# Kernel optimization log

Measured on AMD Instinct MI355X. Metric: run time of the kernel, lower is better.

## Reference

```python
import jax, jax.numpy as jnp
import numpy as np

GRID_ROWS, GRID_COLS = 7, 10
GRID_SIZE = GRID_ROWS * GRID_COLS  # 70
CONTEXT_SIZE = 24
STATE_SIZE = GRID_SIZE + CONTEXT_SIZE  # 94
H = 128  # LSTM_HIDDEN


def setup_inputs() -> dict:
    key = jax.random.key(0)
    ks = jax.random.split(key, 16)
    B, T = 1024, 128
    inp = {
        'states_seq': jax.random.normal(ks[0], (B, T, STATE_SIZE), jnp.float32),
        'actions_seq': jax.random.randint(ks[1], (B, T), 0, 4).astype(jnp.int32),
        # conv params (OIHW)
        'conv1_w': jax.random.normal(ks[2], (16, 1, 3, 3), jnp.float32) * 0.3,
        'conv1_b': jnp.zeros((16,), jnp.float32),
        'conv2_w': jax.random.normal(ks[3], (32, 16, 3, 3), jnp.float32) * 0.08,
        'conv2_b': jnp.zeros((32,), jnp.float32),
        # dense params (out, in) like torch Linear
        'grid_fc_w': jax.random.normal(ks[4], (128, 32 * GRID_SIZE), jnp.float32) * 0.02,
        'grid_fc_b': jnp.zeros((128,), jnp.float32),
        'ctx_fc_w': jax.random.normal(ks[5], (64, CONTEXT_SIZE), jnp.float32) * 0.2,
        'ctx_fc_b': jnp.zeros((64,), jnp.float32),
        'trunk_w': jax.random.normal(ks[6], (128, 192), jnp.float32) * 0.07,
        'trunk_b': jnp.zeros((128,), jnp.float32),
        # LSTM params
        'W_ih': jax.random.normal(ks[7], (4 * H, 128), jnp.float32) * 0.09,
        'b_ih': jnp.zeros((4 * H,), jnp.float32),
        'W_hh': jax.random.normal(ks[8], (4 * H, H), jnp.float32) * 0.09,
        # heads
        'actor_w': jax.random.uniform(ks[9], (4, H), jnp.float32, -0.01, 0.01),
        'actor_b': jnp.zeros((4,), jnp.float32),
        'critic_w': jax.random.uniform(ks[10], (1, H), jnp.float32, -0.01, 0.01),
        'critic_b': jnp.zeros((1,), jnp.float32),
    }
    return inp


def _forward(states_seq, actions_seq, conv1_w, conv1_b, conv2_w, conv2_b,
             grid_fc_w, grid_fc_b, ctx_fc_w, ctx_fc_b, trunk_w, trunk_b,
             W_ih, b_ih, W_hh, actor_w, actor_b, critic_w, critic_b):
    B, T, _ = states_seq.shape
    x = states_seq.reshape(-1, STATE_SIZE)                  # (N, 94)
    grid = x[:, :GRID_SIZE].reshape(-1, 1, GRID_ROWS, GRID_COLS)
    ctx = x[:, GRID_SIZE:]
    g = jax.lax.conv_general_dilated(grid, conv1_w, (1, 1), 'SAME',
                                     dimension_numbers=('NCHW', 'OIHW', 'NCHW'))
    g = jax.nn.relu(g + conv1_b[None, :, None, None])
    g = jax.lax.conv_general_dilated(g, conv2_w, (1, 1), 'SAME',
                                     dimension_numbers=('NCHW', 'OIHW', 'NCHW'))
    g = jax.nn.relu(g + conv2_b[None, :, None, None])
    g = g.reshape(g.shape[0], -1)                           # (N, 2240)
    g = jax.nn.relu(g @ grid_fc_w.T + grid_fc_b)            # (N, 128)
    c = jax.nn.relu(ctx @ ctx_fc_w.T + ctx_fc_b)            # (N, 64)
    trunk = jax.nn.relu(jnp.concatenate([g, c], -1) @ trunk_w.T + trunk_b)
    trunk = trunk.reshape(B, T, 128)

    # LSTM: precompute input-to-gate GEMM for all timesteps, scan over time
    gates_x = jnp.einsum('btd,gd->tbg', trunk, W_ih) + b_ih  # (T, B, 4H)

    def step(carry, gx):
        h, cst = carry
        gates = gx + h @ W_hh.T
        i, f, gg, o = jnp.split(gates, 4, axis=-1)
        i, f, o = jax.nn.sigmoid(i), jax.nn.sigmoid(f), jax.nn.sigmoid(o)
        gg = jnp.tanh(gg)
        cst = f * cst + i * gg
        h = o * jnp.tanh(cst)
        return (h, cst), h

    h0 = jnp.zeros((B, H), trunk.dtype)
    _, hs = jax.lax.scan(step, (h0, h0), gates_x)            # hs: (T, B, H)
    h_flat = jnp.transpose(hs, (1, 0, 2)).reshape(B * T, H)

    logits = h_flat @ actor_w.T + actor_b                    # (N, 4)
    values = (h_flat @ critic_w.T + critic_b)[:, 0]          # (N,)
    logp = jax.nn.log_softmax(logits, axis=-1)
    a = actions_seq.reshape(-1)
    log_probs = jnp.take_along_axis(logp, a[:, None].astype(jnp.int32), axis=-1)[:, 0]
    entropy = -jnp.sum(jnp.exp(logp) * logp, axis=-1)
    return log_probs, values, entropy


def reference(states_seq, actions_seq, conv1_w, conv1_b, conv2_w, conv2_b,
              grid_fc_w, grid_fc_b, ctx_fc_w, ctx_fc_b, trunk_w, trunk_b,
              W_ih, b_ih, W_hh, actor_w, actor_b, critic_w, critic_b):
    return _forward(states_seq, actions_seq, conv1_w, conv1_b, conv2_w, conv2_b,
                    grid_fc_w, grid_fc_b, ctx_fc_w, ctx_fc_b, trunk_w, trunk_b,
                    W_ih, b_ih, W_hh, actor_w, actor_b, critic_w, critic_b)
```

## Files before the change

### kernel.cpp

```cpp
#include <hip/hip_runtime.h>
#include <hip/hip_bf16.h>

typedef unsigned int  u32;
typedef unsigned short u16;
typedef unsigned long long u64;
typedef __attribute__((ext_vector_type(8))) short bf16x8;
typedef __attribute__((ext_vector_type(4))) float f32x4;

#define B_   1024
#define T_   128
#define NBT  (B_*T_)
#define CH   16384
#define NCH  8

#define WG_OFF   0
#define WT_OFF   286720
#define WIH_OFF  311296
#define W2_OFF   376832
#define W1C_OFF  381952
#define CVT_TOTAL 382464

#define TRUNK_OFF (1ull<<20)
#define H_OFF     (36ull<<20)
#define CTX_OFF   (72ull<<20)
#define C2A_OFF   (92ull<<20)
#define C2B_OFF   (C2A_OFF + 74ull*1024*1024)

__device__ __forceinline__ u16 f2bf(float f){
  __hip_bfloat16 h = __float2bfloat16(f);
  return *reinterpret_cast<u16*>(&h);
}
__device__ __forceinline__ float bf2f(u16 u){ return __uint_as_float((u32)u << 16); }
__device__ __forceinline__ float sigm(float x){ return 1.f / (1.f + __expf(-x)); }
__device__ __forceinline__ float tanh_f(float x){ return 2.f / (1.f + __expf(-2.f*x)) - 1.f; }

__device__ __forceinline__ void bar_lds() {
  __builtin_amdgcn_sched_barrier(0);
  asm volatile("s_waitcnt lgkmcnt(0)" ::: "memory");
  __builtin_amdgcn_s_barrier();
  __builtin_amdgcn_sched_barrier(0);
}

__global__ void k_cvt(const float* __restrict__ gfw, const float* __restrict__ tw,
                      const float* __restrict__ wih, const float* __restrict__ c2w,
                      const float* __restrict__ c1w, u16* __restrict__ wsb) {
  int i = blockIdx.x * 256 + threadIdx.x;
  if (i >= CVT_TOTAL) return;
  float v;
  if (i < WT_OFF) {
    int o = i / 2240; int k = i - o*2240;
    int pos = k >> 5, ch = k & 31;
    v = gfw[o*2240 + ch*70 + pos];
  }
  else if (i < WIH_OFF)  v = tw[i - WT_OFF];
  else if (i < W2_OFF)   v = wih[i - WIH_OFF];
  else if (i < W1C_OFF) {
    int j = i - W2_OFF; int co = j / 160; int k = j - co*160;
    int tap = k >> 4; int ci = k & 15;
    v = (tap < 9) ? c2w[co*144 + ci*9 + tap] : 0.f;
  } else {
    int j = i - W1C_OFF; int ch = j >> 5; int k = j & 31;
    v = (k < 9) ? c1w[ch*9 + k] : 0.f;
  }
  wsb[i] = f2bf(v);
}

__device__ void conv_body(char* smem,
    const float* __restrict__ states_c,
    const float* __restrict__ c1b, const float* __restrict__ c2b,
    const float* __restrict__ cfw, const float* __restrict__ cfb,
    const u16* __restrict__ wsb,
    u16* __restrict__ c2buf, u16* __restrict__ ctx_c, int blk)
{
  float (*s_st)[96] = (float(*)[96])smem;
  u16* act1 = (u16*)(smem + 3072);

  const int tid  = threadIdx.x;
  const int lane = tid & 63;
  const int w    = tid >> 6;
  const int arow = lane & 15;
  const int grp  = lane >> 4;
  const int g0   = blk * 64;

  bf16x8 Bc1 = *(const bf16x8*)(wsb + W1C_OFF + arow*32 + grp*8);
  bf16x8 b2f[5][2];
  #pragma unroll
  for (int p = 0; p < 5; p++)
    #pragma unroll
    for (int nt = 0; nt < 2; nt++)
      b2f[p][nt] = *(const bf16x8*)(wsb + W2_OFF + (nt*16 + arow)*160 + p*32 + grp*8);
  float c1bv[4], c2bv0[4], c2bv1[4];
  #pragma unroll
  for (int r = 0; r < 4; r++) {
    c1bv[r]  = c1b[grp*4 + r];
    c2bv0[r] = c2b[grp*4 + r];
    c2bv1[r] = c2b[16 + grp*4 + r];
  }
  const float cfbr = cfb[lane];
  float cfwr[24];
  #pragma unroll
  for (int k = 0; k < 24; k++) cfwr[k] = cfw[lane*24 + k];

  const int sst_s = (tid*2)/94, sst_c = (tid*2)%94;

  if (tid < 376) {
    float2 v = *(const float2*)(states_c + (size_t)g0*94 + tid*2);
    *(float2*)&s_st[sst_s][sst_c] = v;
  }
  for (int i = tid; i < 608; i += 512) {
    int s = i / 76; int r = i - s*76; int hi2 = r >> 1; int h = r & 1;
    int hp;
    if (hi2 < 12)      hp = hi2;
    else if (hi2 < 24) hp = 96 + (hi2 - 12);
    else if (hi2 < 31) hp = (hi2 - 23) * 12;
    else               hp = (hi2 - 30) * 12 + 11;
    u32 a = (u32)((s*108 + hp)*32 + h*16) ^ (u32)((hp & 7) << 4);
    *(uint4*)(act1 ? (char*)act1 + a : 0) = (uint4){0,0,0,0};
  }
  bar_lds();

  const bf16x8 zv = {0,0,0,0,0,0,0,0};

  for (int g = 0; g < 8; g++) {
    const int m0 = g0 + g*8;
    float2 npre;
    const bool haspre = (g < 7) && (tid < 376);
    if (haspre)
      npre = *(const float2*)(states_c + (size_t)(m0 + 8)*94 + tid*2);

    for (int mt = w; mt < 35; mt += 8) {
      int row = mt*16 + arow;
      int s = (int)(((u32)row * 59919u) >> 22); int pos = row - s*70;
      int y = (int)(((u32)pos * 6554u) >> 16);  int x = pos - y*10;
      bf16x8 pf = zv;
      if (grp == 0) {
        const float* gs = &s_st[s][0];
        #pragma unroll
        for (int t = 0; t < 8; t++) {
          int dy = t/3, dx = t - (t/3)*3;
          int yy = y + dy - 1, xx = x + dx - 1;
          bool ok = (yy >= 0) & (yy < 7) & (xx >= 0) & (xx < 10);
          float v = gs[ok ? yy*10 + xx : 0];
          pf[t] = (short)f2bf(ok ? v : 0.f);
        }
      } else if (grp == 1) {
        int yy = y + 1, xx = x + 1;
        bool ok = (yy < 7) & (xx < 10);
        float v = s_st[s][ok ? yy*10 + xx : 0];
        pf[0] = (short)f2bf(ok ? v : 0.f);
      }
      f32x4 acc = __builtin_amdgcn_mfma_f32_16x16x32_bf16(Bc1, pf, (f32x4){0.f,0.f,0.f,0.f}, 0, 0, 0);
      int hp = (y+1)*12 + (x+1);
      u16 q0 = f2bf(fmaxf(acc[0] + c1bv[0], 0.f));
      u16 q1 = f2bf(fmaxf(acc[1] + c1bv[1], 0.f));
      u16 q2 = f2bf(fmaxf(acc[2] + c1bv[2], 0.f));
      u16 q3 = f2bf(fmaxf(acc[3] + c1bv[3], 0.f));
      u64 pk = (u64)q0 | ((u64)q1 << 16) | ((u64)q2 << 32) | ((u64)q3 << 48);
      u32 wa = (u32)(((s*108 + hp)*16 + grp*4)*2) ^ (u32)((hp & 7) << 4);
      *(u64*)((char*)act1 + wa) = pk;
    }
    bar_lds();

    for (int mt = w; mt < 35; mt += 8) {
      int row = mt*16 + arow;
      int s = (int)(((u32)row * 59919u) >> 22); int pos = row - s*70;
      int y = (int)(((u32)pos * 6554u) >> 16);  int x = pos - y*10;
      f32x4 acc0 = {0.f,0.f,0.f,0.f}, acc1 = {0.f,0.f,0.f,0.f};
      #pragma unroll
      for (int p = 0; p < 5; p++) {
        int tap = p*2 + (grp >> 1); if (tap > 8) tap = 8;
        int dy = (tap * 11) >> 5; int dx = tap - dy*3;
        int hp = (y + dy)*12 + (x + dx);
        u32 ra = (u32)(((s*108 + hp)*16 + (grp & 1)*8)*2) ^ (u32)((hp & 7) << 4);
        bf16x8 bv = *(const bf16x8*)((const char*)act1 + ra);
        acc0 = __builtin_amdgcn_mfma_f32_16x16x32_bf16(b2f[p][0], bv, acc0, 0, 0, 0);
        acc1 = __builtin_amdgcn_mfma_f32_16x16x32_bf16(b2f[p][1], bv, acc1, 0, 0, 0);
      }
      {
        u16 q0 = f2bf(fmaxf(acc0[0] + c2bv0[0], 0.f));
        u16 q1 = f2bf(fmaxf(acc0[1] + c2bv0[1], 0.f));
        u16 q2 = f2bf(fmaxf(acc0[2] + c2bv0[2], 0.f));
        u16 q3 = f2bf(fmaxf(acc0[3] + c2bv0[3], 0.f));
        u64 pk = (u64)q0 | ((u64)q1 << 16) | ((u64)q2 << 32) | ((u64)q3 << 48);
        *(u64*)(c2buf + (size_t)(m0 + s)*2240 + pos*32 + grp*4) = pk;
      }
      {
        u16 q0 = f2bf(fmaxf(acc1[0] + c2bv1[0], 0.f));
        u16 q1 = f2bf(fmaxf(acc1[1] + c2bv1[1], 0.f));
        u16 q2 = f2bf(fmaxf(acc1[2] + c2bv1[2], 0.f));
        u16 q3 = f2bf(fmaxf(acc1[3] + c2bv1[3], 0.f));
        u64 pk = (u64)q0 | ((u64)q1 << 16) | ((u64)q2 << 32) | ((u64)q3 << 48);
        *(u64*)(c2buf + (size_t)(m0 + s)*2240 + pos*32 + 16 + grp*4) = pk;
      }
    }
    {
      float a = cfbr;
      #pragma unroll
      for (int k = 0; k < 24; k++) a = fmaf(cfwr[k], s_st[w][70 + k], a);
      ctx_c[(size_t)(m0 + w)*64 + lane] = f2bf(fmaxf(a, 0.f));
    }

    if (g < 7) {
      bar_lds();
      if (haspre) *(float2*)&s_st[sst_s][sst_c] = npre;
      bar_lds();
    }
  }
}

__device__ void gemm_body(char* smem,
    const u16* __restrict__ c2buf, const u16* __restrict__ ctx_c,
    const float* __restrict__ gfb, const float* __restrict__ tbv,
    const u16* __restrict__ wsb, u16* __restrict__ trunk_ws,
    int nbase, int blk)
{
  u16* s_b = (u16*)smem;
  u16* s_g = (u16*)(smem + 36864);

  const int tid  = threadIdx.x;
  const int lane = tid & 63;
  const int w    = tid >> 6;
  const int arow = lane & 15;
  const int grp  = lane >> 4;
  const int wm   = w & 3;
  const int wn   = w >> 2;
  const int m0   = blk * 64;

  float gfbv[4], tbvv[4];
  #pragma unroll
  for (int q = 0; q < 4; q++) {
    gfbv[q] = gfb[(wn*4 + q)*16 + arow];
    tbvv[q] = tbv[(wn*4 + q)*16 + arow];
  }

  const int srow = tid >> 2, sseg = (tid & 3) * 16;
  const u16* wg = wsb + WG_OFF;
  const u16* ap = c2buf + (size_t)(m0 + wm*16 + arow) * 2240 + grp*8;

  {
    const u16* src = wg + (size_t)srow*2240 + sseg;
    *(uint4*)&s_b[srow*72 + sseg]     = *(const uint4*)src;
    *(uint4*)&s_b[srow*72 + sseg + 8] = *(const uint4*)(src + 8);
  }
  bf16x8 aC0 = *(const bf16x8*)(ap);
  bf16x8 aC1 = *(const bf16x8*)(ap + 32);
  bf16x8 aN0 = *(const bf16x8*)(ap + 64);
  bf16x8 aN1 = *(const bf16x8*)(ap + 96);
  f32x4 acc[4];
  #pragma unroll
  for (int q = 0; q < 4; q++) acc[q] = (f32x4){0.f,0.f,0.f,0.f};
  __syncthreads();

  for (int kp = 0; kp < 35; kp++) {
    uint4 b0v, b1v;
    if (kp < 34) {
      const u16* src = wg + (size_t)srow*2240 + (kp+1)*64 + sseg;
      b0v = *(const uint4*)src;
      b1v = *(const uint4*)(src + 8);
    }
    bf16x8 aF0 = aN0, aF1 = aN1;
    if (kp < 33) {
      aF0 = *(const bf16x8*)(ap + (size_t)(kp+2)*64);
      aF1 = *(const bf16x8*)(ap + (size_t)(kp+2)*64 + 32);
    }
    const u16* sb = &s_b[(kp & 1)*9216];
    #pragma unroll
    for (int q = 0; q < 4; q++) {
      bf16x8 bv0 = *(const bf16x8*)&sb[((wn*4 + q)*16 + arow)*72 + grp*8];
      acc[q] = __builtin_amdgcn_mfma_f32_16x16x32_bf16(aC0, bv0, acc[q], 0, 0, 0);
    }
    #pragma unroll
    for (int q = 0; q < 4; q++) {
      bf16x8 bv1 = *(const bf16x8*)&sb[((wn*4 + q)*16 + arow)*72 + 32 + grp*8];
      acc[q] = __builtin_amdgcn_mfma_f32_16x16x32_bf16(aC1, bv1, acc[q], 0, 0, 0);
    }
    if (kp < 34) {
      *(uint4*)&s_b[((kp+1) & 1)*9216 + srow*72 + sseg]     = b0v;
      *(uint4*)&s_b[((kp+1) & 1)*9216 + srow*72 + sseg + 8] = b1v;
    }
    aC0 = aN0; aC1 = aN1; aN0 = aF0; aN1 = aF1;
    bar_lds();
  }

  #pragma unroll
  for (int q = 0; q < 4; q++)
    #pragma unroll
    for (int r = 0; r < 4; r++)
      s_g[(wm*16 + grp*4 + r)*204 + (wn*4 + q)*16 + arow] = f2bf(fmaxf(acc[q][r] + gfbv[q], 0.f));
  {
    int row = tid >> 3, seg = (tid & 7) * 8;
    uint4 c0 = *(const uint4*)(ctx_c + (size_t)(m0 + row)*64 + seg);
    *(uint4*)&s_g[row*204 + 128 + seg] = c0;
  }
  bar_lds();

  f32x4 tacc[4];
  #pragma unroll
  for (int q = 0; q < 4; q++) tacc[q] = (f32x4){0.f,0.f,0.f,0.f};
  #pragma unroll
  for (int ks = 0; ks < 6; ks++) {
    bf16x8 av = *(const bf16x8*)&s_g[(wm*16 + arow)*204 + ks*32 + grp*8];
    #pragma unroll
    for (int q = 0; q < 4; q++) {
      bf16x8 bv = *(const bf16x8*)(wsb + WT_OFF + (size_t)((wn*4 + q)*16 + arow)*192 + ks*32 + grp*8);
      tacc[q] = __builtin_amdgcn_mfma_f32_16x16x32_bf16(av, bv, tacc[q], 0, 0, 0);
    }
  }
  bar_lds();
  #pragma unroll
  for (int q = 0; q < 4; q++)
    #pragma unroll
    for (int r = 0; r < 4; r++)
      s_g[(wm*16 + grp*4 + r)*204 + (wn*4 + q)*16 + arow] = f2bf(fmaxf(tacc[q][r] + tbvv[q], 0.f));
  bar_lds();

  {
    const int t0 = (nbase + m0) & 127;
    const int bb = (nbase + m0) >> 7;
    int row = tid >> 3, seg = (tid & 7) * 16;
    #pragma unroll
    for (int j = 0; j < 2; j++) {
      uint4 v = *(const uint4*)&s_g[row*204 + seg + j*8];
      *(uint4*)(trunk_ws + ((size_t)(t0 + row)*B_ + bb)*128 + seg + j*8) = v;
    }
  }
}

__global__ __launch_bounds__(512, 2) void k_fused(
    const float* __restrict__ states,
    const float* __restrict__ c1b, const float* __restrict__ c2b,
    const float* __restrict__ cfw, const float* __restrict__ cfb,
    const float* __restrict__ gfb, const float* __restrict__ tbv,
    const u16* __restrict__ wsb,
    u16* __restrict__ c2a, u16* __restrict__ c2bb,
    u16* __restrict__ ctxg, u16* __restrict__ trunk_ws,
    int i, int nconv)
{
  __shared__ __align__(16) char smem[62976];
  if ((int)blockIdx.x < nconv) {
    const float* st_c = states + (size_t)i * CH * 94;
    u16* c2w_  = (i & 1) ? c2bb : c2a;
    u16* ctx_c = ctxg + (size_t)i * CH * 64;
    conv_body(smem, st_c, c1b, c2b, cfw, cfb, wsb, c2w_, ctx_c, blockIdx.x);
  } else {
    const int c = i - 1;
    const u16* c2r   = (c & 1) ? c2bb : c2a;
    const u16* ctx_c = ctxg + (size_t)c * CH * 64;
    gemm_body(smem, c2r, ctx_c, gfb, tbv, wsb, trunk_ws, c*CH, blockIdx.x - nconv);
  }
}

__global__ __launch_bounds__(512, 1) void k_lstm(
    const u16* __restrict__ trunk_ws, const float* __restrict__ whh,
    const float* __restrict__ wih, const float* __restrict__ bih,
    u16* __restrict__ h_ws)
{
  __shared__ __align__(16) u16 s_h[2][16*136];
  __shared__ __align__(16) u16 s_tk[3][4*136];

  const int tid  = threadIdx.x;
  const int lane = tid & 63;
  const int w    = tid >> 6;
  const int arow = lane & 15;
  const int grp  = lane >> 4;
  const int b0   = blockIdx.x * 4;

  bf16x8 Bv[4][4], Bw[4][4];
  float bihv[4];
  #pragma unroll
  for (int j = 0; j < 4; j++) {
    const int row = j*128 + w*16 + arow;
    bihv[j] = bih[row];
    #pragma unroll
    for (int ks = 0; ks < 4; ks++) {
      const float* s1 = whh + (size_t)row*128 + ks*32 + grp*8;
      const float* s2 = wih + (size_t)row*128 + ks*32 + grp*8;
      float4 a0 = *(const float4*)s1, a1 = *(const float4*)(s1 + 4);
      float4 b0v = *(const float4*)s2, b1v = *(const float4*)(s2 + 4);
      bf16x8 t1, t2;
      t1[0]=(short)f2bf(a0.x); t1[1]=(short)f2bf(a0.y); t1[2]=(short)f2bf(a0.z); t1[3]=(short)f2bf(a0.w);
      t1[4]=(short)f2bf(a1.x); t1[5]=(short)f2bf(a1.y); t1[6]=(short)f2bf(a1.z); t1[7]=(short)f2bf(a1.w);
      t2[0]=(short)f2bf(b0v.x); t2[1]=(short)f2bf(b0v.y); t2[2]=(short)f2bf(b0v.z); t2[3]=(short)f2bf(b0v.w);
      t2[4]=(short)f2bf(b1v.x); t2[5]=(short)f2bf(b1v.y); t2[6]=(short)f2bf(b1v.z); t2[7]=(short)f2bf(b1v.w);
      Bv[j][ks] = t1; Bw[j][ks] = t2;
    }
  }

  for (int i = tid; i < 2*16*136; i += 512) ((u16*)s_h)[i] = 0;

  const int prow = tid >> 4, pseg = (tid & 15) * 8;
  if (tid < 64) {
    #pragma unroll
    for (int s = 0; s < 3; s++)
      *(uint4*)&s_tk[s][prow*136 + pseg] =
          *(const uint4*)(trunk_ws + ((size_t)s*B_ + b0 + prow)*128 + pseg);
  }
  uint4 P0 = {0,0,0,0};
  if (tid < 64)
    P0 = *(const uint4*)(trunk_ws + ((size_t)3*B_ + b0 + prow)*128 + pseg);

  float cst = 0.f;
  __syncthreads();

  f32x4 xA[4];
  #pragma unroll
  for (int j = 0; j < 4; j++) xA[j] = (f32x4){0.f,0.f,0.f,0.f};
  #pragma unroll
  for (int ks = 0; ks < 4; ks++) {
    bf16x8 av = *(const bf16x8*)&s_tk[0][(arow & 3)*136 + ks*32 + grp*8];
    #pragma unroll
    for (int j = 0; j < 4; j++)
      xA[j] = __builtin_amdgcn_mfma_f32_16x16x32_bf16(av, Bw[j][ks], xA[j], 0, 0, 0);
  }

  for (int t = 0; t < T_; t++) {
    const int p = t & 1;

    uint4 P1 = {0,0,0,0};
    if ((t + 4 < T_) && tid < 64)
      P1 = *(const uint4*)(trunk_ws + ((size_t)(t+4)*B_ + b0 + prow)*128 + pseg);

    if (t > 0 && tid < 64) {
      uint4 hv = *(const uint4*)&s_h[p][prow*136 + pseg];
      *(uint4*)(h_ws + ((size_t)(t-1)*B_ + b0 + prow)*128 + pseg) = hv;
    }

    f32x4 racc[4], xB[4];
    #pragma unroll
    for (int j = 0; j < 4; j++) { racc[j] = (f32x4){0.f,0.f,0.f,0.f}; xB[j] = (f32x4){0.f,0.f,0.f,0.f}; }
    #pragma unroll
    for (int ks = 0; ks < 4; ks++) {
      bf16x8 av = *(const bf16x8*)&s_h[p][arow*136 + ks*32 + grp*8];
      #pragma unroll
      for (int j = 0; j < 4; j++)
        racc[j] = __builtin_amdgcn_mfma_f32_16x16x32_bf16(av, Bv[j][ks], racc[j], 0, 0, 0);
    }
    {
      const u16* tk = &s_tk[(t+1) % 3][0];
      #pragma unroll
      for (int ks = 0; ks < 4; ks++) {
        bf16x8 av = *(const bf16x8*)&tk[(arow & 3)*136 + ks*32 + grp*8];
        #pragma unroll
        for (int j = 0; j < 4; j++)
          xB[j] = __builtin_amdgcn_mfma_f32_16x16x32_bf16(av, Bw[j][ks], xB[j], 0, 0, 0);
      }
    }

    float g4[4];
    #pragma unroll
    for (int j = 0; j < 4; j++) {
      float s0 = racc[j][0] + xA[j][0];
      float s1 = racc[j][1] + xA[j][1];
      float s2 = racc[j][2] + xA[j][2];
      float s3 = racc[j][3] + xA[j][3];
      float t0v = __shfl(s0, arow);
      float t1v = __shfl(s1, arow);
      float t2v = __shfl(s2, arow);
      float t3v = __shfl(s3, arow);
      g4[j] = (grp == 0) ? t0v : (grp == 1) ? t1v : (grp == 2) ? t2v : t3v;
    }

    {
      float xi = g4[0] + bihv[0];
      float xf = g4[1] + bihv[1];
      float xg = g4[2] + bihv[2];
      float xo = g4[3] + bihv[3];
      float I = sigm(xi), F = sigm(xf), O = sigm(xo), G = tanh_f(xg);
      cst = F*cst + I*G;
      float hvv = O * tanh_f(cst);
      s_h[1-p][grp*136 + w*16 + arow] = f2bf(hvv);
    }

    if ((t + 3 < T_) && tid < 64)
      *(uint4*)&s_tk[t % 3][prow*136 + pseg] = P0;
    P0 = P1;
    #pragma unroll
    for (int j = 0; j < 4; j++) xA[j] = xB[j];
    bar_lds();
  }

  if (tid < 64) {
    uint4 hv = *(const uint4*)&s_h[T_ & 1][prow*136 + pseg];
    *(uint4*)(h_ws + ((size_t)(T_-1)*B_ + b0 + prow)*128 + pseg) = hv;
  }
}

__global__ __launch_bounds__(256, 1) void k_heads(
    const u16* __restrict__ h_ws, const int* __restrict__ actions,
    const float* __restrict__ aw, const float* __restrict__ ab,
    const float* __restrict__ cw, const float* __restrict__ cb,
    float* __restrict__ out)
{
  const int tid  = threadIdx.x;
  const int lane = tid & 63;
  const int w    = tid >> 6;
  const int arow = lane & 15;
  const int grp  = lane >> 4;

  bf16x8 Ah[4];
  #pragma unroll
  for (int ks = 0; ks < 4; ks++) {
    bf16x8 v = {0,0,0,0,0,0,0,0};
    if (arow < 4) {
      const float* src = aw + arow*128 + ks*32 + grp*8;
      #pragma unroll
      for (int j = 0; j < 8; j++) v[j] = (short)f2bf(src[j]);
    } else if (arow == 4) {
      const float* src = cw + ks*32 + grp*8;
      #pragma unroll
      for (int j = 0; j < 8; j++) v[j] = (short)f2bf(src[j]);
    }
    Ah[ks] = v;
  }
  const float ab0=ab[0], ab1=ab[1], ab2=ab[2], ab3=ab[3], cb0=cb[0];

  #pragma unroll
  for (int g = 0; g < 4; g++) {
    int m0 = (blockIdx.x*4 + w)*64 + g*16;
    int t  = m0 >> 10; int bb = m0 & 1023;
    f32x4 acc = {0.f,0.f,0.f,0.f};
    #pragma unroll
    for (int ks = 0; ks < 4; ks++) {
      bf16x8 bv = *(const bf16x8*)(h_ws + ((size_t)t*B_ + bb + arow)*128 + ks*32 + grp*8);
      acc = __builtin_amdgcn_mfma_f32_16x16x32_bf16(Ah[ks], bv, acc, 0, 0, 0);
    }
    float cr = __shfl_xor(acc[0], 16);
    if (grp == 0) {
      float L0 = acc[0] + ab0, L1 = acc[1] + ab1, L2 = acc[2] + ab2, L3 = acc[3] + ab3;
      float Lv = cr + cb0;
      float mm = fmaxf(fmaxf(L0, L1), fmaxf(L2, L3));
      float e0 = __expf(L0-mm), e1 = __expf(L1-mm), e2 = __expf(L2-mm), e3 = __expf(L3-mm);
      float S = e0+e1+e2+e3; float lse = __logf(S);
      float p0=L0-mm-lse, p1=L1-mm-lse, p2=L2-mm-lse, p3=L3-mm-lse;
      int n = (bb + arow)*T_ + t;
      int a = actions[n];
      float lpa = (a==0)?p0:(a==1)?p1:(a==2)?p2:p3;
      float ent = -(e0*p0 + e1*p1 + e2*p2 + e3*p3) / S;
      out[n] = lpa; out[NBT + n] = Lv; out[2*NBT + n] = ent;
    }
  }
}

extern "C" void kernel_launch(void* const* d_in, const int* in_sizes, int n_in,
                              void* d_out, int out_size, void* d_ws, size_t ws_size,
                              hipStream_t stream) {
  const float* states = (const float*)d_in[0];
  const int*   actions= (const int*)  d_in[1];
  const float* c1w = (const float*)d_in[2];
  const float* c1b = (const float*)d_in[3];
  const float* c2w = (const float*)d_in[4];
  const float* c2b = (const float*)d_in[5];
  const float* gfw = (const float*)d_in[6];
  const float* gfb = (const float*)d_in[7];
  const float* cfw = (const float*)d_in[8];
  const float* cfb = (const float*)d_in[9];
  const float* tw  = (const float*)d_in[10];
  const float* tbv = (const float*)d_in[11];
  const float* wih = (const float*)d_in[12];
  const float* bih = (const float*)d_in[13];
  const float* whh = (const float*)d_in[14];
  const float* aw  = (const float*)d_in[15];
  const float* ab  = (const float*)d_in[16];
  const float* cw  = (const float*)d_in[17];
  const float* cb  = (const float*)d_in[18];
  float* out = (float*)d_out;

  u16* wsb   = (u16*)d_ws;
  u16* trunk = (u16*)((char*)d_ws + TRUNK_OFF);
  u16* h_ws  = (u16*)((char*)d_ws + H_OFF);
  u16* ctxg  = (u16*)((char*)d_ws + CTX_OFF);
  u16* c2a   = (u16*)((char*)d_ws + C2A_OFF);
  u16* c2bb  = (u16*)((char*)d_ws + C2B_OFF);

  k_cvt<<<(CVT_TOTAL + 255)/256, 256, 0, stream>>>(gfw, tw, wih, c2w, c1w, wsb);

  for (int i = 0; i <= NCH; i++) {
    const int nconv = (i < NCH) ? (CH/64) : 0;
    const int ngemm = (i > 0)   ? (CH/64) : 0;
    k_fused<<<nconv + ngemm, 512, 0, stream>>>(states, c1b, c2b, cfw, cfb,
                                               gfb, tbv, wsb, c2a, c2bb,
                                               ctxg, trunk, i, nconv);
  }
  k_lstm<<<B_/4, 512, 0, stream>>>(trunk, whh, wih, bih, h_ws);
  k_heads<<<512, 256, 0, stream>>>(h_ws, actions, aw, ab, cw, cb, out);
}
```

Before: 784.7 us.

## Fuse conv and grid GEMM per block, enlarge chunks, pad LSTM LDS rows

Replaces the software-pipelined launch sequence, where each launch ran the conv for chunk i and the GEMM for chunk i-1 in separate blocks using double-buffered conv2 scratch, with a kernel in which each block runs conv and then immediately runs the GEMM on its own rows. A threadfence and syncthreads separate the two phases. Chunks double in size, giving fewer launches, and the conv2 buffer becomes single. The LSTM shared-memory row stride changes from 136 to 144 elements, which alters the LDS bank mapping. The design assumes each block's GEMM reads only the conv output that same block produced; otherwise the result is racy. The conv2 intermediate, now twice as large per chunk, may also be less likely to stay in cache.

```diff
diff --git a/kernel.cpp b/kernel.cpp
--- a/kernel.cpp
+++ b/kernel.cpp
@@ -10,8 +10,8 @@
 #define B_   1024
 #define T_   128
 #define NBT  (B_*T_)
-#define CH   16384
-#define NCH  8
+#define CHUNK 32768
+#define NCHUNK 4
 
 #define WG_OFF   0
 #define WT_OFF   286720
@@ -23,8 +23,7 @@
 #define TRUNK_OFF (1ull<<20)
 #define H_OFF     (36ull<<20)
 #define CTX_OFF   (72ull<<20)
-#define C2A_OFF   (92ull<<20)
-#define C2B_OFF   (C2A_OFF + 74ull*1024*1024)
+#define C2_OFF    (92ull<<20)
 
 __device__ __forceinline__ u16 f2bf(float f){
   __hip_bfloat16 h = __float2bfloat16(f);
@@ -115,7 +114,7 @@
     else if (hi2 < 31) hp = (hi2 - 23) * 12;
     else               hp = (hi2 - 30) * 12 + 11;
     u32 a = (u32)((s*108 + hp)*32 + h*16) ^ (u32)((hp & 7) << 4);
-    *(uint4*)(act1 ? (char*)act1 + a : 0) = (uint4){0,0,0,0};
+    *(uint4*)((char*)act1 + a) = (uint4){0,0,0,0};
   }
   bar_lds();
 
@@ -326,28 +325,22 @@
   }
 }
 
-__global__ __launch_bounds__(512, 2) void k_fused(
+__global__ __launch_bounds__(512, 2) void k_cg(
     const float* __restrict__ states,
     const float* __restrict__ c1b, const float* __restrict__ c2b,
     const float* __restrict__ cfw, const float* __restrict__ cfb,
     const float* __restrict__ gfb, const float* __restrict__ tbv,
     const u16* __restrict__ wsb,
-    u16* __restrict__ c2a, u16* __restrict__ c2bb,
-    u16* __restrict__ ctxg, u16* __restrict__ trunk_ws,
-    int i, int nconv)
+    u16* __restrict__ c2g, u16* __restrict__ ctxg,
+    u16* __restrict__ trunk_ws, int c)
 {
   __shared__ __align__(16) char smem[62976];
-  if ((int)blockIdx.x < nconv) {
-    const float* st_c = states + (size_t)i * CH * 94;
-    u16* c2w_  = (i & 1) ? c2bb : c2a;
-    u16* ctx_c = ctxg + (size_t)i * CH * 64;
-    conv_body(smem, st_c, c1b, c2b, cfw, cfb, wsb, c2w_, ctx_c, blockIdx.x);
-  } else {
-    const int c = i - 1;
-    const u16* c2r   = (c & 1) ? c2bb : c2a;
-    const u16* ctx_c = ctxg + (size_t)c * CH * 64;
-    gemm_body(smem, c2r, ctx_c, gfb, tbv, wsb, trunk_ws, c*CH, blockIdx.x - nconv);
-  }
+  const float* st_c  = states + (size_t)c * CHUNK * 94;
+  u16*         ctx_c = ctxg + (size_t)c * CHUNK * 64;
+  conv_body(smem, st_c, c1b, c2b, cfw, cfb, wsb, c2g, ctx_c, blockIdx.x);
+  __threadfence();
+  __syncthreads();
+  gemm_body(smem, c2g, ctx_c, gfb, tbv, wsb, trunk_ws, c*CHUNK, blockIdx.x);
 }
 
 __global__ __launch_bounds__(512, 1) void k_lstm(
@@ -355,8 +348,8 @@
     const float* __restrict__ wih, const float* __restrict__ bih,
     u16* __restrict__ h_ws)
 {
-  __shared__ __align__(16) u16 s_h[2][16*136];
-  __shared__ __align__(16) u16 s_tk[3][4*136];
+  __shared__ __align__(16) u16 s_h[2][16*144];
+  __shared__ __align__(16) u16 s_tk[3][4*144];
 
   const int tid  = threadIdx.x;
   const int lane = tid & 63;
@@ -386,13 +379,13 @@
     }
   }
 
-  for (int i = tid; i < 2*16*136; i += 512) ((u16*)s_h)[i] = 0;
+  for (int i = tid; i < 2*16*144; i += 512) ((u16*)s_h)[i] = 0;
 
   const int prow = tid >> 4, pseg = (tid & 15) * 8;
   if (tid < 64) {
     #pragma unroll
     for (int s = 0; s < 3; s++)
-      *(uint4*)&s_tk[s][prow*136 + pseg] =
+      *(uint4*)&s_tk[s][prow*144 + pseg] =
           *(const uint4*)(trunk_ws + ((size_t)s*B_ + b0 + prow)*128 + pseg);
   }
   uint4 P0 = {0,0,0,0};
@@ -407,7 +400,7 @@
   for (int j = 0; j < 4; j++) xA[j] = (f32x4){0.f,0.f,0.f,0.f};
   #pragma unroll
   for (int ks = 0; ks < 4; ks++) {
-    bf16x8 av = *(const bf16x8*)&s_tk[0][(arow & 3)*136 + ks*32 + grp*8];
+    bf16x8 av = *(const bf16x8*)&s_tk[0][(arow & 3)*144 + ks*32 + grp*8];
     #pragma unroll
     for (int j = 0; j < 4; j++)
       xA[j] = __builtin_amdgcn_mfma_f32_16x16x32_bf16(av, Bw[j][ks], xA[j], 0, 0, 0);
@@ -421,7 +414,7 @@
       P1 = *(const uint4*)(trunk_ws + ((size_t)(t+4)*B_ + b0 + prow)*128 + pseg);
 
     if (t > 0 && tid < 64) {
-      uint4 hv = *(const uint4*)&s_h[p][prow*136 + pseg];
+      uint4 hv = *(const uint4*)&s_h[p][prow*144 + pseg];
       *(uint4*)(h_ws + ((size_t)(t-1)*B_ + b0 + prow)*128 + pseg) = hv;
     }
 
@@ -430,7 +423,7 @@
     for (int j = 0; j < 4; j++) { racc[j] = (f32x4){0.f,0.f,0.f,0.f}; xB[j] = (f32x4){0.f,0.f,0.f,0.f}; }
     #pragma unroll
     for (int ks = 0; ks < 4; ks++) {
-      bf16x8 av = *(const bf16x8*)&s_h[p][arow*136 + ks*32 + grp*8];
+      bf16x8 av = *(const bf16x8*)&s_h[p][arow*144 + ks*32 + grp*8];
       #pragma unroll
       for (int j = 0; j < 4; j++)
         racc[j] = __builtin_amdgcn_mfma_f32_16x16x32_bf16(av, Bv[j][ks], racc[j], 0, 0, 0);
@@ -439,7 +432,7 @@
       const u16* tk = &s_tk[(t+1) % 3][0];
       #pragma unroll
       for (int ks = 0; ks < 4; ks++) {
-        bf16x8 av = *(const bf16x8*)&tk[(arow & 3)*136 + ks*32 + grp*8];
+        bf16x8 av = *(const bf16x8*)&tk[(arow & 3)*144 + ks*32 + grp*8];
         #pragma unroll
         for (int j = 0; j < 4; j++)
           xB[j] = __builtin_amdgcn_mfma_f32_16x16x32_bf16(av, Bw[j][ks], xB[j], 0, 0, 0);
@@ -468,11 +461,11 @@
       float I = sigm(xi), F = sigm(xf), O = sigm(xo), G = tanh_f(xg);
       cst = F*cst + I*G;
       float hvv = O * tanh_f(cst);
-      s_h[1-p][grp*136 + w*16 + arow] = f2bf(hvv);
+      s_h[1-p][grp*144 + w*16 + arow] = f2bf(hvv);
     }
 
     if ((t + 3 < T_) && tid < 64)
-      *(uint4*)&s_tk[t % 3][prow*136 + pseg] = P0;
+      *(uint4*)&s_tk[t % 3][prow*144 + pseg] = P0;
     P0 = P1;
     #pragma unroll
     for (int j = 0; j < 4; j++) xA[j] = xB[j];
@@ -480,7 +473,7 @@
   }
 
   if (tid < 64) {
-    uint4 hv = *(const uint4*)&s_h[T_ & 1][prow*136 + pseg];
+    uint4 hv = *(const uint4*)&s_h[T_ & 1][prow*144 + pseg];
     *(uint4*)(h_ws + ((size_t)(T_-1)*B_ + b0 + prow)*128 + pseg) = hv;
   }
 }
@@ -569,17 +562,13 @@
   u16* trunk = (u16*)((char*)d_ws + TRUNK_OFF);
   u16* h_ws  = (u16*)((char*)d_ws + H_OFF);
   u16* ctxg  = (u16*)((char*)d_ws + CTX_OFF);
-  u16* c2a   = (u16*)((char*)d_ws + C2A_OFF);
-  u16* c2bb  = (u16*)((char*)d_ws + C2B_OFF);
+  u16* c2g   = (u16*)((char*)d_ws + C2_OFF);
 
   k_cvt<<<(CVT_TOTAL + 255)/256, 256, 0, stream>>>(gfw, tw, wih, c2w, c1w, wsb);
 
-  for (int i = 0; i <= NCH; i++) {
-    const int nconv = (i < NCH) ? (CH/64) : 0;
-    const int ngemm = (i > 0)   ? (CH/64) : 0;
-    k_fused<<<nconv + ngemm, 512, 0, stream>>>(states, c1b, c2b, cfw, cfb,
-                                               gfb, tbv, wsb, c2a, c2bb,
-                                               ctxg, trunk, i, nconv);
+  for (int c = 0; c < NCHUNK; c++) {
+    k_cg<<<CHUNK/64, 512, 0, stream>>>(states, c1b, c2b, cfw, cfb,
+                                       gfb, tbv, wsb, c2g, ctxg, trunk, c);
   }
   k_lstm<<<B_/4, 512, 0, stream>>>(trunk, whh, wih, bih, h_ws);
   k_heads<<<512, 256, 0, stream>>>(h_ws, actions, aw, ab, cw, cb, out);
```

After: 1.210 ms. 1.54x slower.
